# Optimization experiments

Hardware: AMD Instinct MI355X
Metric: run time of the kernel (lower is better)

Reference implementation:

```python
import jax, jax.numpy as jnp
import numpy as np

T, K, D_SLOTS, D_IN, D_HID, EPSILON = 3, 11, 64, 128, 256, 1e-8


def _layer_norm(x, g, b, eps=1e-5):
    m = jnp.mean(x, axis=-1, keepdims=True)
    v = jnp.mean((x - m) ** 2, axis=-1, keepdims=True)
    return (x - m) * jax.lax.rsqrt(v + eps) * g + b


def _gru_cell(x, h, w_ih, w_hh, b_ih, b_hh):
    # torch.nn.GRUCell math; w_ih/w_hh stored as [D, 3D] (input-major)
    gx = x @ w_ih + b_ih
    gh = h @ w_hh + b_hh
    xr, xz, xn = jnp.split(gx, 3, axis=-1)
    hr, hz, hn = jnp.split(gh, 3, axis=-1)
    r = jax.nn.sigmoid(xr + hr)
    z = jax.nn.sigmoid(xz + hz)
    n = jnp.tanh(xn + r * hn)
    return (1.0 - z) * n + z * h


def setup_inputs() -> dict:
    key = jax.random.key(0)
    ks = jax.random.split(key, 12)
    B, N = 64, 4096
    s = 0.02
    return {
        "inputs": jax.random.normal(ks[0], (B, N, D_IN), jnp.float32),
        "ln_in_g": jnp.ones((D_IN,), jnp.float32),
        "ln_in_b": jnp.zeros((D_IN,), jnp.float32),
        "Wk": jax.random.normal(ks[1], (D_IN, D_SLOTS), jnp.float32) * s,
        "Wv": jax.random.normal(ks[2], (D_IN, D_SLOTS), jnp.float32) * s,
        "init_latents": jax.random.normal(ks[3], (1, K, D_SLOTS), jnp.float32),
        "ln_q_g": jnp.ones((D_SLOTS,), jnp.float32),
        "ln_q_b": jnp.zeros((D_SLOTS,), jnp.float32),
        "Wq": jax.random.normal(ks[4], (D_SLOTS, D_SLOTS), jnp.float32) * s,
        "w_ih": jax.random.normal(ks[5], (D_SLOTS, 3 * D_SLOTS), jnp.float32) * s,
        "w_hh": jax.random.normal(ks[6], (D_SLOTS, 3 * D_SLOTS), jnp.float32) * s,
        "b_ih": jnp.zeros((3 * D_SLOTS,), jnp.float32),
        "b_hh": jnp.zeros((3 * D_SLOTS,), jnp.float32),
        "ln_f_g": jnp.ones((D_SLOTS,), jnp.float32),
        "ln_f_b": jnp.zeros((D_SLOTS,), jnp.float32),
        "W1": jax.random.normal(ks[7], (D_SLOTS, D_HID), jnp.float32) * s,
        "b1": jnp.zeros((D_HID,), jnp.float32),
        "W2": jax.random.normal(ks[8], (D_HID, D_SLOTS), jnp.float32) * s,
        "b2": jnp.zeros((D_SLOTS,), jnp.float32),
    }


def reference(inputs, ln_in_g, ln_in_b, Wk, Wv, init_latents, ln_q_g, ln_q_b, Wq,
              w_ih, w_hh, b_ih, b_hh, ln_f_g, ln_f_b, W1, b1, W2, b2):
    B = inputs.shape[0]
    x = _layer_norm(inputs, ln_in_g, ln_in_b)          # [B,N,128]
    keys = x @ Wk                                       # [B,N,D]
    vals = x @ Wv                                       # [B,N,D]
    slots = jnp.broadcast_to(init_latents, (B, K, D_SLOTS))
    scale = D_SLOTS ** (-0.5)
    attn2 = None
    for _ in range(T):
        slots_prev = slots
        q = _layer_norm(slots, ln_q_g, ln_q_b) @ Wq     # [B,K,D]
        logits = scale * jnp.einsum('bnc,bmc->bnm', keys, q)  # [B,N,K]
        attn = jax.nn.softmax(logits, axis=-1) + EPSILON
        attn2 = attn
        attn_n = attn / jnp.sum(attn, axis=1, keepdims=True)   # competing norm over inputs
        updates = jnp.einsum('bnm,bnc->bmc', attn_n, vals)     # [B,K,D]
        slots = _gru_cell(updates.reshape(B * K, D_SLOTS),
                          slots_prev.reshape(B * K, D_SLOTS),
                          w_ih, w_hh, b_ih, b_hh).reshape(B, K, D_SLOTS)
        h = jax.nn.relu(_layer_norm(slots, ln_f_g, ln_f_b) @ W1 + b1)
        slots = slots + (h @ W2 + b2)
    return slots, attn2
```

## Files before the change

### kernel.cpp

```cpp
#include <hip/hip_runtime.h>

#define DIN   128
#define DSL   64
#define KSL   11
#define NTOK  4096
#define NB    64
#define NSPLIT 64
#define LN_EPS   1e-5f
#define ATTN_EPS 1e-8f
#define SCALE    0.125f

typedef __bf16 bf16x8 __attribute__((ext_vector_type(8)));
typedef float  f32x4  __attribute__((ext_vector_type(4)));

__global__ void k_prep(const float* __restrict__ Wk, const float* __restrict__ Wv,
                       __bf16* __restrict__ WTf) {
  const int t = blockIdx.x * 256 + threadIdx.x;
  const int fid = t >> 6, lane = t & 63;
  const int ks = fid >> 3, nt = fid & 7;
  const int col = nt * 16 + (lane & 15);
  const int kb  = ks * 32 + (lane >> 4) * 8;
  union { uint4 u; __bf16 h[8]; } o;
#pragma unroll
  for (int j = 0; j < 8; ++j) {
    const int k = kb + j;
    const float v = (col < 64) ? Wk[k * 64 + col] : Wv[k * 64 + (col - 64)];
    o.h[j] = (__bf16)v;
  }
  *((uint4*)WTf + t) = o.u;
}

__launch_bounds__(256)
__global__ void k_lnproj(const float* __restrict__ inp, const float* __restrict__ g,
                         const float* __restrict__ bb, const __bf16* __restrict__ WTf,
                         __bf16* __restrict__ keys, __bf16* __restrict__ valsT) {
  __shared__ __bf16 Xs[4][16][136];
  const int tid = threadIdx.x, wave = tid >> 6, lane = tid & 63;
  const int half = lane >> 5, hl = lane & 31;
  const int rbase = blockIdx.x * 64 + wave * 16;

  const float4 gv = *(const float4*)(g + hl * 4);
  const float4 bv = *(const float4*)(bb + hl * 4);

  float4 xr[8];
#pragma unroll
  for (int p = 0; p < 8; ++p)
    xr[p] = *(const float4*)(inp + (size_t)(rbase + 2 * p + half) * DIN + hl * 4);
  __builtin_amdgcn_sched_barrier(0);

  float s[8], sq[8];
#pragma unroll
  for (int p = 0; p < 8; ++p) {
    s[p]  = xr[p].x + xr[p].y + xr[p].z + xr[p].w;
    sq[p] = xr[p].x * xr[p].x + xr[p].y * xr[p].y + xr[p].z * xr[p].z + xr[p].w * xr[p].w;
  }
#pragma unroll
  for (int o = 16; o > 0; o >>= 1) {
#pragma unroll
    for (int p = 0; p < 8; ++p) { s[p] += __shfl_xor(s[p], o); sq[p] += __shfl_xor(sq[p], o); }
  }
#pragma unroll
  for (int p = 0; p < 8; ++p) {
    const float m = s[p] * (1.f / 128.f);
    const float rstd = rsqrtf(sq[p] * (1.f / 128.f) - m * m + LN_EPS);
    union { ushort4 u; __bf16 h[4]; } pk;
    pk.h[0] = (__bf16)((xr[p].x - m) * rstd * gv.x + bv.x);
    pk.h[1] = (__bf16)((xr[p].y - m) * rstd * gv.y + bv.y);
    pk.h[2] = (__bf16)((xr[p].z - m) * rstd * gv.z + bv.z);
    pk.h[3] = (__bf16)((xr[p].w - m) * rstd * gv.w + bv.w);
    *(ushort4*)&Xs[wave][2 * p + half][hl * 4] = pk.u;
  }

  f32x4 acc[8] = {};
  const int tok = lane & 15, kgrp = lane >> 4;
  const bf16x8* __restrict__ Bv = (const bf16x8*)WTf;
#pragma unroll
  for (int ks = 0; ks < 4; ++ks) {
    const bf16x8 x = *(const bf16x8*)&Xs[wave][tok][ks * 32 + kgrp * 8];
#pragma unroll
    for (int nt = 0; nt < 8; ++nt) {
      const bf16x8 w = Bv[(ks * 8 + nt) * 64 + lane];
      acc[nt] = __builtin_amdgcn_mfma_f32_16x16x32_bf16(w, x, acc[nt], 0, 0, 0);
    }
  }
#pragma unroll
  for (int nt = 0; nt < 4; ++nt) {
    union { unsigned long long u; __bf16 h[4]; } pk;
    pk.h[0] = (__bf16)acc[nt][0]; pk.h[1] = (__bf16)acc[nt][1];
    pk.h[2] = (__bf16)acc[nt][2]; pk.h[3] = (__bf16)acc[nt][3];
    *(unsigned long long*)&keys[(size_t)(rbase + tok) * 64 + nt * 16 + kgrp * 4] = pk.u;
  }
  const int bidx = rbase >> 12;
  const int tIB  = (rbase & 4095) + tok;
#pragma unroll
  for (int nt = 4; nt < 8; ++nt) {
#pragma unroll
    for (int r = 0; r < 4; ++r)
      valsT[((size_t)bidx * 64 + (nt - 4) * 16 + kgrp * 4 + r) * NTOK + tIB] = (__bf16)acc[nt][r];
  }
}

__global__ void k_init(const float* __restrict__ init_lat, const float* __restrict__ qg,
                       const float* __restrict__ qb, const float* __restrict__ Wq,
                       float* __restrict__ slots, float* __restrict__ q) {
  const int b = blockIdx.x;
  const int k = threadIdx.x >> 6, c = threadIdx.x & 63;
  const float s = init_lat[k * DSL + c];
  slots[(size_t)(b * KSL + k) * DSL + c] = s;
  float sum = s, sq = s * s;
#pragma unroll
  for (int o = 32; o > 0; o >>= 1) { sum += __shfl_xor(sum, o); sq += __shfl_xor(sq, o); }
  const float m = sum * (1.f / 64.f);
  const float rstd = rsqrtf(sq * (1.f / 64.f) - m * m + LN_EPS);
  const float qn = (s - m) * rstd * qg[c] + qb[c];
  float acc = 0.f;
  for (int i = 0; i < DSL; ++i) acc += __shfl(qn, i) * Wq[i * DSL + c];
  q[(size_t)(b * KSL + k) * DSL + c] = acc;
}

__launch_bounds__(64)
__global__ void k_attn(const __bf16* __restrict__ keys, const __bf16* __restrict__ valsT,
                       const float* __restrict__ q, float* __restrict__ Upart,
                       float* __restrict__ Spart, float* __restrict__ attn_out) {
  __shared__ __bf16 P[16][72];
  const int b = blockIdx.x >> 6, sp = blockIdx.x & 63;
  const int lane = threadIdx.x;
  const int g = lane >> 4, t = lane & 15;

  bf16x8 qf[2];
#pragma unroll
  for (int ks = 0; ks < 2; ++ks) {
    float4 q0 = {0.f, 0.f, 0.f, 0.f}, q1 = {0.f, 0.f, 0.f, 0.f};
    if (t < KSL) {
      const float* __restrict__ qp = q + (size_t)(b * KSL + t) * DSL + ks * 32 + g * 8;
      q0 = *(const float4*)qp; q1 = *(const float4*)(qp + 4);
    }
    qf[ks][0] = (__bf16)q0.x; qf[ks][1] = (__bf16)q0.y;
    qf[ks][2] = (__bf16)q0.z; qf[ks][3] = (__bf16)q0.w;
    qf[ks][4] = (__bf16)q1.x; qf[ks][5] = (__bf16)q1.y;
    qf[ks][6] = (__bf16)q1.z; qf[ks][7] = (__bf16)q1.w;
  }

  const __bf16* __restrict__ kbase = keys + ((size_t)b * NTOK + sp * 64) * DSL;
  float sacc[4] = {0.f, 0.f, 0.f, 0.f};

#pragma unroll
  for (int tile = 0; tile < 4; ++tile) {
    f32x4 c = {};
#pragma unroll
    for (int ks = 0; ks < 2; ++ks) {
      const bf16x8 kf = *(const bf16x8*)(kbase + (size_t)(tile * 16 + t) * DSL + ks * 32 + g * 8);
      c = __builtin_amdgcn_mfma_f32_16x16x32_bf16(qf[ks], kf, c, 0, 0, 0);
    }
    float lg[4];
#pragma unroll
    for (int r = 0; r < 4; ++r)
      lg[r] = (4 * g + r < KSL) ? c[r] * SCALE : -1e30f;
    float mx = fmaxf(fmaxf(lg[0], lg[1]), fmaxf(lg[2], lg[3]));
    mx = fmaxf(mx, __shfl_xor(mx, 16));
    mx = fmaxf(mx, __shfl_xor(mx, 32));
    float e[4];
#pragma unroll
    for (int r = 0; r < 4; ++r) e[r] = __expf(lg[r] - mx);
    float se = e[0] + e[1] + e[2] + e[3];
    se += __shfl_xor(se, 16);
    se += __shfl_xor(se, 32);
    const float inv = 1.f / se;
#pragma unroll
    for (int r = 0; r < 4; ++r) {
      const float a = e[r] * inv + ATTN_EPS;
      sacc[r] += a;
      P[4 * g + r][tile * 16 + t] = (__bf16)a;
      if (attn_out && 4 * g + r < KSL)
        attn_out[((size_t)b * NTOK + sp * 64 + tile * 16 + t) * KSL + 4 * g + r] = a;
    }
  }

  f32x4 U[4] = {};
#pragma unroll
  for (int ks = 0; ks < 2; ++ks) {
    const bf16x8 pf = *(const bf16x8*)&P[t][ks * 32 + g * 8];
#pragma unroll
    for (int ct = 0; ct < 4; ++ct) {
      const bf16x8 vf = *(const bf16x8*)(valsT + ((size_t)b * DSL + ct * 16 + t) * NTOK
                                         + sp * 64 + ks * 32 + g * 8);
      U[ct] = __builtin_amdgcn_mfma_f32_16x16x32_bf16(pf, vf, U[ct], 0, 0, 0);
    }
  }
  float* __restrict__ up = Upart + (size_t)(b * NSPLIT + sp) * (KSL * DSL);
#pragma unroll
  for (int ct = 0; ct < 4; ++ct)
#pragma unroll
    for (int r = 0; r < 4; ++r)
      if (4 * g + r < KSL) up[(4 * g + r) * DSL + ct * 16 + t] = U[ct][r];

#pragma unroll
  for (int r = 0; r < 4; ++r) {
#pragma unroll
    for (int o = 1; o < 16; o <<= 1) sacc[r] += __shfl_xor(sacc[r], o);
  }
  if (t == 0) {
    float* __restrict__ spp = Spart + (size_t)(b * NSPLIT + sp) * 16;
#pragma unroll
    for (int r = 0; r < 4; ++r) spp[4 * g + r] = sacc[r];
  }
}

__launch_bounds__(64)
__global__ void k_update(const float* __restrict__ Upart, const float* __restrict__ Spart,
                         float* __restrict__ slots, const float* __restrict__ w_ih,
                         const float* __restrict__ w_hh, const float* __restrict__ b_ih,
                         const float* __restrict__ b_hh, const float* __restrict__ fg,
                         const float* __restrict__ fb, const float* __restrict__ W1,
                         const float* __restrict__ b1v, const float* __restrict__ W2,
                         const float* __restrict__ b2v, const float* __restrict__ qg,
                         const float* __restrict__ qbv, const float* __restrict__ Wq,
                         float* __restrict__ q, float* __restrict__ out_slots) {
  const int row = blockIdx.x;
  const int c = threadIdx.x;
  const int b = row / 11, k = row - b * 11;

  float u = 0.f;
  for (int s = 0; s < NSPLIT; ++s)
    u += Upart[((size_t)(b * NSPLIT + s) * KSL + k) * DSL + c];
  float ss = 0.f;
  for (int s = 0; s < NSPLIT; ++s)
    ss += Spart[(size_t)(b * NSPLIT + s) * 16 + k];
  u /= ss;

  const float h = slots[(size_t)row * DSL + c];

  float gr = b_ih[c], gz = b_ih[64 + c], gn = b_ih[128 + c];
  float hr = b_hh[c], hz = b_hh[64 + c], hn = b_hh[128 + c];
  for (int i = 0; i < 64; ++i) {
    const float ui = __shfl(u, i), hi = __shfl(h, i);
    gr += ui * w_ih[i * 192 + c];       hr += hi * w_hh[i * 192 + c];
    gz += ui * w_ih[i * 192 + 64 + c];  hz += hi * w_hh[i * 192 + 64 + c];
    gn += ui * w_ih[i * 192 + 128 + c]; hn += hi * w_hh[i * 192 + 128 + c];
  }
  const float r = 1.f / (1.f + __expf(-(gr + hr)));
  const float z = 1.f / (1.f + __expf(-(gz + hz)));
  const float nn = tanhf(gn + r * hn);
  float sv = (1.f - z) * nn + z * h;

  float sum = sv, sq = sv * sv;
#pragma unroll
  for (int o = 32; o > 0; o >>= 1) { sum += __shfl_xor(sum, o); sq += __shfl_xor(sq, o); }
  float m = sum * (1.f / 64.f);
  float rstd = rsqrtf(sq * (1.f / 64.f) - m * m + LN_EPS);
  const float sl = (sv - m) * rstd * fg[c] + fb[c];

  float h0 = b1v[c], h1 = b1v[64 + c], h2 = b1v[128 + c], h3 = b1v[192 + c];
  for (int i = 0; i < 64; ++i) {
    const float si = __shfl(sl, i);
    h0 += si * W1[i * 256 + c];        h1 += si * W1[i * 256 + 64 + c];
    h2 += si * W1[i * 256 + 128 + c];  h3 += si * W1[i * 256 + 192 + c];
  }
  h0 = fmaxf(h0, 0.f); h1 = fmaxf(h1, 0.f); h2 = fmaxf(h2, 0.f); h3 = fmaxf(h3, 0.f);

  float o = b2v[c];
  for (int j = 0; j < 64; ++j) o += __shfl(h0, j) * W2[j * DSL + c];
  for (int j = 0; j < 64; ++j) o += __shfl(h1, j) * W2[(64 + j) * DSL + c];
  for (int j = 0; j < 64; ++j) o += __shfl(h2, j) * W2[(128 + j) * DSL + c];
  for (int j = 0; j < 64; ++j) o += __shfl(h3, j) * W2[(192 + j) * DSL + c];
  sv += o;

  slots[(size_t)row * DSL + c] = sv;
  if (out_slots) out_slots[(size_t)row * DSL + c] = sv;

  float s2 = sv, q2 = sv * sv;
#pragma unroll
  for (int o2 = 32; o2 > 0; o2 >>= 1) { s2 += __shfl_xor(s2, o2); q2 += __shfl_xor(q2, o2); }
  m = s2 * (1.f / 64.f);
  rstd = rsqrtf(q2 * (1.f / 64.f) - m * m + LN_EPS);
  const float qn = (sv - m) * rstd * qg[c] + qbv[c];
  float qa = 0.f;
  for (int i = 0; i < 64; ++i) qa += __shfl(qn, i) * Wq[i * DSL + c];
  q[(size_t)row * DSL + c] = qa;
}

extern "C" void kernel_launch(void* const* d_in, const int* in_sizes, int n_in,
                              void* d_out, int out_size, void* d_ws, size_t ws_size,
                              hipStream_t stream) {
  const float* inp  = (const float*)d_in[0];
  const float* lng  = (const float*)d_in[1];
  const float* lnb  = (const float*)d_in[2];
  const float* Wk   = (const float*)d_in[3];
  const float* Wv   = (const float*)d_in[4];
  const float* init = (const float*)d_in[5];
  const float* qg   = (const float*)d_in[6];
  const float* qbb  = (const float*)d_in[7];
  const float* Wq   = (const float*)d_in[8];
  const float* wih  = (const float*)d_in[9];
  const float* whh  = (const float*)d_in[10];
  const float* bih  = (const float*)d_in[11];
  const float* bhh  = (const float*)d_in[12];
  const float* fg   = (const float*)d_in[13];
  const float* fb   = (const float*)d_in[14];
  const float* W1   = (const float*)d_in[15];
  const float* b1   = (const float*)d_in[16];
  const float* W2   = (const float*)d_in[17];
  const float* b2   = (const float*)d_in[18];

  char* wsb = (char*)d_ws;
  __bf16* keys  = (__bf16*)wsb;
  __bf16* valsT = keys + (size_t)NB * NTOK * DSL;
  __bf16* WTf   = valsT + (size_t)NB * DSL * NTOK;
  float* slots = (float*)(WTf + 16384);
  float* q     = slots + NB * KSL * DSL;
  float* Upart = q + NB * KSL * DSL;
  float* Spart = Upart + (size_t)NB * NSPLIT * KSL * DSL;

  float* out_slots = (float*)d_out;
  float* out_attn  = (float*)d_out + NB * KSL * DSL;

  k_prep<<<8, 256, 0, stream>>>(Wk, Wv, WTf);
  k_lnproj<<<4096, 256, 0, stream>>>(inp, lng, lnb, WTf, keys, valsT);
  k_init<<<NB, KSL * 64, 0, stream>>>(init, qg, qbb, Wq, slots, q);
  for (int t = 0; t < 3; ++t) {
    k_attn<<<NB * NSPLIT, 64, 0, stream>>>(keys, valsT, q, Upart, Spart,
                                           t == 2 ? out_attn : nullptr);
    k_update<<<NB * KSL, 64, 0, stream>>>(Upart, Spart, slots, wih, whh, bih, bhh,
                                          fg, fb, W1, b1, W2, b2, qg, qbb, Wq, q,
                                          t == 2 ? out_slots : nullptr);
  }
}
```

Measured before the change: 188.5 us.

## Fold layernorm affine into projection weights, halve attention splits, prefold scale

The input layernorm's gain is folded into the bf16 K/V weights, and its mean, rstd and bias are applied after the MFMA through precomputed column sums of the weights. This lets the raw inputs be converted to bf16 without waiting on the row reductions. Weight fragments are now prefetched one k-step ahead in the projection. The attention kernel handles 128 tokens per block (NSPLIT 32), which halves the partial writes, and the softmax scale moves into q. Converting raw inputs to bf16 before centring may lose accuracy when row means are large.

```diff
diff --git a/kernel.cpp b/kernel.cpp
--- a/kernel.cpp
+++ b/kernel.cpp
@@ -5,7 +5,7 @@
 #define KSL   11
 #define NTOK  4096
 #define NB    64
-#define NSPLIT 64
+#define NSPLIT 32
 #define LN_EPS   1e-5f
 #define ATTN_EPS 1e-8f
 #define SCALE    0.125f
@@ -14,7 +14,22 @@
 typedef float  f32x4  __attribute__((ext_vector_type(4)));
 
 __global__ void k_prep(const float* __restrict__ Wk, const float* __restrict__ Wv,
-                       __bf16* __restrict__ WTf) {
+                       const float* __restrict__ g, const float* __restrict__ b,
+                       __bf16* __restrict__ WTf, float* __restrict__ EP) {
+  if (blockIdx.x == 8) {
+    const int c = threadIdx.x;
+    if (c < 128) {
+      const float* __restrict__ W = (c < 64) ? Wk : Wv;
+      const int cc = c & 63;
+      float G = 0.f, Bt = 0.f;
+      for (int k = 0; k < 128; ++k) {
+        const float w = W[k * 64 + cc];
+        G += g[k] * w; Bt += b[k] * w;
+      }
+      EP[c] = G; EP[128 + c] = Bt;
+    }
+    return;
+  }
   const int t = blockIdx.x * 256 + threadIdx.x;
   const int fid = t >> 6, lane = t & 63;
   const int ks = fid >> 3, nt = fid & 7;
@@ -24,79 +39,95 @@
 #pragma unroll
   for (int j = 0; j < 8; ++j) {
     const int k = kb + j;
-    const float v = (col < 64) ? Wk[k * 64 + col] : Wv[k * 64 + (col - 64)];
+    const float v = ((col < 64) ? Wk[k * 64 + col] : Wv[k * 64 + (col - 64)]) * g[k];
     o.h[j] = (__bf16)v;
   }
   *((uint4*)WTf + t) = o.u;
 }
 
 __launch_bounds__(256)
-__global__ void k_lnproj(const float* __restrict__ inp, const float* __restrict__ g,
-                         const float* __restrict__ bb, const __bf16* __restrict__ WTf,
-                         __bf16* __restrict__ keys, __bf16* __restrict__ valsT) {
+__global__ void k_lnproj(const float* __restrict__ inp, const __bf16* __restrict__ WTf,
+                         const float* __restrict__ EP, __bf16* __restrict__ keys,
+                         __bf16* __restrict__ valsT) {
   __shared__ __bf16 Xs[4][16][136];
+  __shared__ float rowstats[4][16][2];
   const int tid = threadIdx.x, wave = tid >> 6, lane = tid & 63;
   const int half = lane >> 5, hl = lane & 31;
+  const int t = lane & 15, g = lane >> 4;
   const int rbase = blockIdx.x * 64 + wave * 16;
-
-  const float4 gv = *(const float4*)(g + hl * 4);
-  const float4 bv = *(const float4*)(bb + hl * 4);
 
   float4 xr[8];
 #pragma unroll
   for (int p = 0; p < 8; ++p)
     xr[p] = *(const float4*)(inp + (size_t)(rbase + 2 * p + half) * DIN + hl * 4);
-  __builtin_amdgcn_sched_barrier(0);
 
   float s[8], sq[8];
 #pragma unroll
   for (int p = 0; p < 8; ++p) {
     s[p]  = xr[p].x + xr[p].y + xr[p].z + xr[p].w;
     sq[p] = xr[p].x * xr[p].x + xr[p].y * xr[p].y + xr[p].z * xr[p].z + xr[p].w * xr[p].w;
-  }
+    union { ushort4 u; __bf16 h[4]; } pk;
+    pk.h[0] = (__bf16)xr[p].x; pk.h[1] = (__bf16)xr[p].y;
+    pk.h[2] = (__bf16)xr[p].z; pk.h[3] = (__bf16)xr[p].w;
+    *(ushort4*)&Xs[wave][2 * p + half][hl * 4] = pk.u;
+  }
+
 #pragma unroll
   for (int o = 16; o > 0; o >>= 1) {
 #pragma unroll
     for (int p = 0; p < 8; ++p) { s[p] += __shfl_xor(s[p], o); sq[p] += __shfl_xor(sq[p], o); }
   }
-#pragma unroll
-  for (int p = 0; p < 8; ++p) {
+  if (hl < 8) {
+    const int p = hl;
     const float m = s[p] * (1.f / 128.f);
     const float rstd = rsqrtf(sq[p] * (1.f / 128.f) - m * m + LN_EPS);
-    union { ushort4 u; __bf16 h[4]; } pk;
-    pk.h[0] = (__bf16)((xr[p].x - m) * rstd * gv.x + bv.x);
-    pk.h[1] = (__bf16)((xr[p].y - m) * rstd * gv.y + bv.y);
-    pk.h[2] = (__bf16)((xr[p].z - m) * rstd * gv.z + bv.z);
-    pk.h[3] = (__bf16)((xr[p].w - m) * rstd * gv.w + bv.w);
-    *(ushort4*)&Xs[wave][2 * p + half][hl * 4] = pk.u;
-  }
-
+    rowstats[wave][2 * p + half][0] = m;
+    rowstats[wave][2 * p + half][1] = rstd;
+  }
+
+  const bf16x8* __restrict__ Wv8 = (const bf16x8*)WTf;
+  bf16x8 wf[8];
+#pragma unroll
+  for (int nt = 0; nt < 8; ++nt) wf[nt] = Wv8[nt * 64 + lane];
   f32x4 acc[8] = {};
-  const int tok = lane & 15, kgrp = lane >> 4;
-  const bf16x8* __restrict__ Bv = (const bf16x8*)WTf;
 #pragma unroll
   for (int ks = 0; ks < 4; ++ks) {
-    const bf16x8 x = *(const bf16x8*)&Xs[wave][tok][ks * 32 + kgrp * 8];
-#pragma unroll
-    for (int nt = 0; nt < 8; ++nt) {
-      const bf16x8 w = Bv[(ks * 8 + nt) * 64 + lane];
-      acc[nt] = __builtin_amdgcn_mfma_f32_16x16x32_bf16(w, x, acc[nt], 0, 0, 0);
-    }
-  }
-#pragma unroll
-  for (int nt = 0; nt < 4; ++nt) {
-    union { unsigned long long u; __bf16 h[4]; } pk;
-    pk.h[0] = (__bf16)acc[nt][0]; pk.h[1] = (__bf16)acc[nt][1];
-    pk.h[2] = (__bf16)acc[nt][2]; pk.h[3] = (__bf16)acc[nt][3];
-    *(unsigned long long*)&keys[(size_t)(rbase + tok) * 64 + nt * 16 + kgrp * 4] = pk.u;
-  }
+    const bf16x8 xf = *(const bf16x8*)&Xs[wave][t][ks * 32 + g * 8];
+    bf16x8 wn[8];
+    if (ks < 3) {
+#pragma unroll
+      for (int nt = 0; nt < 8; ++nt) wn[nt] = Wv8[((ks + 1) * 8 + nt) * 64 + lane];
+    }
+#pragma unroll
+    for (int nt = 0; nt < 8; ++nt)
+      acc[nt] = __builtin_amdgcn_mfma_f32_16x16x32_bf16(wf[nt], xf, acc[nt], 0, 0, 0);
+#pragma unroll
+    for (int nt = 0; nt < 8; ++nt) wf[nt] = wn[nt];
+  }
+
+  const float2 mrs = *(const float2*)&rowstats[wave][t][0];
+  const float rstd = mrs.y, mm = mrs.x * mrs.y;
   const int bidx = rbase >> 12;
-  const int tIB  = (rbase & 4095) + tok;
-#pragma unroll
-  for (int nt = 4; nt < 8; ++nt) {
-#pragma unroll
-    for (int r = 0; r < 4; ++r)
-      valsT[((size_t)bidx * 64 + (nt - 4) * 16 + kgrp * 4 + r) * NTOK + tIB] = (__bf16)acc[nt][r];
+  const int tIB  = (rbase & 4095) + t;
+#pragma unroll
+  for (int nt = 0; nt < 8; ++nt) {
+    const float4 Gv = *(const float4*)(EP + nt * 16 + g * 4);
+    const float4 Bv = *(const float4*)(EP + 128 + nt * 16 + g * 4);
+    float o0 = rstd * acc[nt][0] - mm * Gv.x + Bv.x;
+    float o1 = rstd * acc[nt][1] - mm * Gv.y + Bv.y;
+    float o2 = rstd * acc[nt][2] - mm * Gv.z + Bv.z;
+    float o3 = rstd * acc[nt][3] - mm * Gv.w + Bv.w;
+    if (nt < 4) {
+      union { unsigned long long u; __bf16 h[4]; } pk;
+      pk.h[0] = (__bf16)o0; pk.h[1] = (__bf16)o1; pk.h[2] = (__bf16)o2; pk.h[3] = (__bf16)o3;
+      *(unsigned long long*)&keys[(size_t)(rbase + t) * 64 + nt * 16 + g * 4] = pk.u;
+    } else {
+      const int vc = (nt - 4) * 16 + g * 4;
+      valsT[((size_t)bidx * 64 + vc + 0) * NTOK + tIB] = (__bf16)o0;
+      valsT[((size_t)bidx * 64 + vc + 1) * NTOK + tIB] = (__bf16)o1;
+      valsT[((size_t)bidx * 64 + vc + 2) * NTOK + tIB] = (__bf16)o2;
+      valsT[((size_t)bidx * 64 + vc + 3) * NTOK + tIB] = (__bf16)o3;
+    }
   }
 }
 
@@ -115,15 +146,15 @@
   const float qn = (s - m) * rstd * qg[c] + qb[c];
   float acc = 0.f;
   for (int i = 0; i < DSL; ++i) acc += __shfl(qn, i) * Wq[i * DSL + c];
-  q[(size_t)(b * KSL + k) * DSL + c] = acc;
+  q[(size_t)(b * KSL + k) * DSL + c] = acc * SCALE;
 }
 
 __launch_bounds__(64)
 __global__ void k_attn(const __bf16* __restrict__ keys, const __bf16* __restrict__ valsT,
                        const float* __restrict__ q, float* __restrict__ Upart,
                        float* __restrict__ Spart, float* __restrict__ attn_out) {
-  __shared__ __bf16 P[16][72];
-  const int b = blockIdx.x >> 6, sp = blockIdx.x & 63;
+  __shared__ __bf16 P[2][16][72];
+  const int b = blockIdx.x >> 5, sp = blockIdx.x & 31;
   const int lane = threadIdx.x;
   const int g = lane >> 4, t = lane & 15;
 
@@ -141,52 +172,57 @@
     qf[ks][6] = (__bf16)q1.z; qf[ks][7] = (__bf16)q1.w;
   }
 
-  const __bf16* __restrict__ kbase = keys + ((size_t)b * NTOK + sp * 64) * DSL;
+  const __bf16* __restrict__ kbase = keys + ((size_t)b * NTOK + sp * 128) * DSL;
   float sacc[4] = {0.f, 0.f, 0.f, 0.f};
-
-#pragma unroll
-  for (int tile = 0; tile < 4; ++tile) {
-    f32x4 c = {};
+  f32x4 U[4] = {};
+
+#pragma unroll
+  for (int gr = 0; gr < 2; ++gr) {
+    const int tb = gr * 64;
+#pragma unroll
+    for (int tile = 0; tile < 4; ++tile) {
+      f32x4 c = {};
+#pragma unroll
+      for (int ks = 0; ks < 2; ++ks) {
+        const bf16x8 kf = *(const bf16x8*)(kbase + (size_t)(tb + tile * 16 + t) * DSL
+                                           + ks * 32 + g * 8);
+        c = __builtin_amdgcn_mfma_f32_16x16x32_bf16(qf[ks], kf, c, 0, 0, 0);
+      }
+      float lg[4];
+#pragma unroll
+      for (int r = 0; r < 4; ++r)
+        lg[r] = (4 * g + r < KSL) ? c[r] : -1e30f;
+      float mx = fmaxf(fmaxf(lg[0], lg[1]), fmaxf(lg[2], lg[3]));
+      mx = fmaxf(mx, __shfl_xor(mx, 16));
+      mx = fmaxf(mx, __shfl_xor(mx, 32));
+      float e[4];
+#pragma unroll
+      for (int r = 0; r < 4; ++r) e[r] = __expf(lg[r] - mx);
+      float se = e[0] + e[1] + e[2] + e[3];
+      se += __shfl_xor(se, 16);
+      se += __shfl_xor(se, 32);
+      const float inv = 1.f / se;
+#pragma unroll
+      for (int r = 0; r < 4; ++r) {
+        const float a = e[r] * inv + ATTN_EPS;
+        sacc[r] += a;
+        P[gr][4 * g + r][tile * 16 + t] = (__bf16)a;
+        if (attn_out && 4 * g + r < KSL)
+          attn_out[((size_t)b * NTOK + sp * 128 + tb + tile * 16 + t) * KSL + 4 * g + r] = a;
+      }
+    }
 #pragma unroll
     for (int ks = 0; ks < 2; ++ks) {
-      const bf16x8 kf = *(const bf16x8*)(kbase + (size_t)(tile * 16 + t) * DSL + ks * 32 + g * 8);
-      c = __builtin_amdgcn_mfma_f32_16x16x32_bf16(qf[ks], kf, c, 0, 0, 0);
-    }
-    float lg[4];
-#pragma unroll
-    for (int r = 0; r < 4; ++r)
-      lg[r] = (4 * g + r < KSL) ? c[r] * SCALE : -1e30f;
-    float mx = fmaxf(fmaxf(lg[0], lg[1]), fmaxf(lg[2], lg[3]));
-    mx = fmaxf(mx, __shfl_xor(mx, 16));
-    mx = fmaxf(mx, __shfl_xor(mx, 32));
-    float e[4];
-#pragma unroll
-    for (int r = 0; r < 4; ++r) e[r] = __expf(lg[r] - mx);
-    float se = e[0] + e[1] + e[2] + e[3];
-    se += __shfl_xor(se, 16);
-    se += __shfl_xor(se, 32);
-    const float inv = 1.f / se;
-#pragma unroll
-    for (int r = 0; r < 4; ++r) {
-      const float a = e[r] * inv + ATTN_EPS;
-      sacc[r] += a;
-      P[4 * g + r][tile * 16 + t] = (__bf16)a;
-      if (attn_out && 4 * g + r < KSL)
-        attn_out[((size_t)b * NTOK + sp * 64 + tile * 16 + t) * KSL + 4 * g + r] = a;
-    }
-  }
-
-  f32x4 U[4] = {};
-#pragma unroll
-  for (int ks = 0; ks < 2; ++ks) {
-    const bf16x8 pf = *(const bf16x8*)&P[t][ks * 32 + g * 8];
-#pragma unroll
-    for (int ct = 0; ct < 4; ++ct) {
-      const bf16x8 vf = *(const bf16x8*)(valsT + ((size_t)b * DSL + ct * 16 + t) * NTOK
-                                         + sp * 64 + ks * 32 + g * 8);
-      U[ct] = __builtin_amdgcn_mfma_f32_16x16x32_bf16(pf, vf, U[ct], 0, 0, 0);
-    }
-  }
+      const bf16x8 pf = *(const bf16x8*)&P[gr][t][ks * 32 + g * 8];
+#pragma unroll
+      for (int ct = 0; ct < 4; ++ct) {
+        const bf16x8 vf = *(const bf16x8*)(valsT + ((size_t)b * DSL + ct * 16 + t) * NTOK
+                                           + sp * 128 + tb + ks * 32 + g * 8);
+        U[ct] = __builtin_amdgcn_mfma_f32_16x16x32_bf16(pf, vf, U[ct], 0, 0, 0);
+      }
+    }
+  }
+
   float* __restrict__ up = Upart + (size_t)(b * NSPLIT + sp) * (KSL * DSL);
 #pragma unroll
   for (int ct = 0; ct < 4; ++ct)
@@ -276,7 +312,7 @@
   const float qn = (sv - m) * rstd * qg[c] + qbv[c];
   float qa = 0.f;
   for (int i = 0; i < 64; ++i) qa += __shfl(qn, i) * Wq[i * DSL + c];
-  q[(size_t)row * DSL + c] = qa;
+  q[(size_t)row * DSL + c] = qa * SCALE;
 }
 
 extern "C" void kernel_launch(void* const* d_in, const int* in_sizes, int n_in,
@@ -306,7 +342,8 @@
   __bf16* keys  = (__bf16*)wsb;
   __bf16* valsT = keys + (size_t)NB * NTOK * DSL;
   __bf16* WTf   = valsT + (size_t)NB * DSL * NTOK;
-  float* slots = (float*)(WTf + 16384);
+  float* EP    = (float*)(WTf + 16384);
+  float* slots = EP + 256;
   float* q     = slots + NB * KSL * DSL;
   float* Upart = q + NB * KSL * DSL;
   float* Spart = Upart + (size_t)NB * NSPLIT * KSL * DSL;
@@ -314,8 +351,8 @@
   float* out_slots = (float*)d_out;
   float* out_attn  = (float*)d_out + NB * KSL * DSL;
 
-  k_prep<<<8, 256, 0, stream>>>(Wk, Wv, WTf);
-  k_lnproj<<<4096, 256, 0, stream>>>(inp, lng, lnb, WTf, keys, valsT);
+  k_prep<<<9, 256, 0, stream>>>(Wk, Wv, lng, lnb, WTf, EP);
+  k_lnproj<<<4096, 256, 0, stream>>>(inp, WTf, EP, keys, valsT);
   k_init<<<NB, KSL * 64, 0, stream>>>(init, qg, qbb, Wq, slots, q);
   for (int t = 0; t < 3; ++t) {
     k_attn<<<NB * NSPLIT, 64, 0, stream>>>(keys, valsT, q, Upart, Spart,
```

Measured after the change: 185.2 us. Within noise of the previous version (-1.7%).
